# Optimization experiments

Hardware: AMD Instinct MI355X
Metric: run time of the kernel (lower is better)

Reference implementation:

```python
import jax, jax.numpy as jnp
import numpy as np

IN_DIM = 4096
OUT_DIM = 4096
R = 8
C = 2
ALPHA = 32.0
RC = R // C  # head dim = 4
SCALING = ALPHA / R


def setup_inputs() -> dict:
    key = jax.random.key(0)
    ks = jax.random.split(key, 8)
    s = lambda k, shape, fan_in: jax.random.normal(k, shape, jnp.float32) / np.sqrt(fan_in)
    return {
        "x": jax.random.normal(ks[0], (4, 2048, IN_DIM), jnp.float32),
        "W_pre": s(ks[1], (OUT_DIM, IN_DIM), IN_DIM),
        "b_pre": jnp.zeros((OUT_DIM,), jnp.float32),
        "W_down": s(ks[2], (R, IN_DIM), IN_DIM),
        "W_qkv": s(ks[3], (3 * RC, R), R),
        "W_o": s(ks[4], (R, RC), RC),
        "W_up": s(ks[5], (OUT_DIM, R), R),
        "diag_b": jnp.full((OUT_DIM,), 0.001, jnp.float32),
    }


def reference(x, W_pre, b_pre, W_down, W_qkv, W_o, W_up, diag_b):
    # pretrained frozen linear
    pretrained_out = jnp.einsum("bsi,oi->bso", x, W_pre) + b_pre
    # adapter path (dropout in eval mode -> identity)
    down = jnp.einsum("bsi,ri->bsr", x, W_down)          # [B,S,R]
    qkv = jnp.einsum("bsr,tr->bst", down, W_qkv)          # [B,S,3*RC]
    q, k, v = jnp.split(qkv, 3, axis=-1)                  # each [B,S,RC]
    scores = jnp.einsum("bqd,bkd->bqk", q, k) / jnp.sqrt(jnp.float32(RC))
    attn = jax.nn.softmax(scores, axis=-1)
    ctx = jnp.einsum("bqk,bkd->bqd", attn, v)             # [B,S,RC]
    o = jnp.einsum("bsd,rd->bsr", ctx, W_o)               # [B,S,R]
    up = jnp.einsum("bsr,or->bso", o, W_up)               # [B,S,OUT]
    return pretrained_out + up * diag_b * SCALING
```

## Files before the change

### kernel.cpp

```cpp
#include <hip/hip_runtime.h>
#include <stdint.h>

#define KDIM 4096
#define NDIM 4096
#define MROWS 8192
#define SEQ 2048

typedef __attribute__((ext_vector_type(8))) short short8;
typedef __attribute__((ext_vector_type(4))) float f32x4;

__device__ __forceinline__ float bf16_bits_to_f(uint32_t u16) {
  union { uint32_t u; float f; } c; c.u = u16 << 16; return c.f;
}
__device__ __forceinline__ float dload(const void* p, size_t idx, int flag) {
  if (flag) return bf16_bits_to_f(((const uint16_t*)p)[idx]);
  return ((const float*)p)[idx];
}
__device__ __forceinline__ uint16_t f2b(float f) {
  union { float f; uint32_t u; } c; c.f = f;
  uint32_t b = c.u;
  return (uint16_t)((b + 0x7FFFu + ((b >> 16) & 1u)) >> 16);
}
__device__ __forceinline__ uint32_t pk2(float a, float b) {
  return (uint32_t)f2b(a) | ((uint32_t)f2b(b) << 16);
}
__device__ __forceinline__ void gld_lds16(const uint16_t* g, uint16_t* l) {
  __builtin_amdgcn_global_load_lds(
      (const __attribute__((address_space(1))) uint32_t*)g,
      (__attribute__((address_space(3))) uint32_t*)l, 16, 0, 0);
}

#define BARRIER() asm volatile("s_barrier" ::: "memory")
#define VMCNT4() asm volatile("s_waitcnt vmcnt(4)" ::: "memory")
#define VMCNT0() asm volatile("s_waitcnt vmcnt(0)" ::: "memory")

__global__ void k_detect(const uint16_t* xu, int* flag) {
  int lane = threadIdx.x;
  int bad = 0;
  for (int i = lane; i < 512; i += 64) {
    float v = bf16_bits_to_f((uint32_t)xu[i]);
    if (!(v == v) || fabsf(v) > 1000.0f) bad++;
  }
  for (int off = 32; off > 0; off >>= 1) bad += __shfl_down(bad, off);
  if (lane == 0) *flag = (bad < 32) ? 1 : 0;
}

__global__ __launch_bounds__(256) void k_prep(
    const void* W_down, const void* W_qkv, const void* W_up,
    const void* diag_b, const void* b_pre,
    float* WcT, float* W_up_s, float* b_pre_f, const int* flagp) {
  const int flag = *flagp;
  const int tid = blockIdx.x * 256 + threadIdx.x;
  const int tt = tid >> 12;
  const int i = tid & 4095;
  float s = 0.f;
#pragma unroll
  for (int r = 0; r < 8; ++r)
    s += dload(W_qkv, tt * 8 + r, flag) * dload(W_down, (size_t)r * 4096 + i, flag);
  WcT[(size_t)tt * 4096 + i] = s;
  if (tid < 32768)
    W_up_s[tid] = dload(W_up, tid, flag) * dload(diag_b, tid >> 3, flag) * 4.0f;
  if (tid < 4096)
    b_pre_f[tid] = dload(b_pre, tid, flag);
}

__global__ __launch_bounds__(256) void k_qkvconv(
    const void* x, const float* WcT, float* qkv, uint16_t* xb,
    const void* W_pre, uint16_t* wb, int do_conv, const int* flagp) {
  const int flag = *flagp;
  if (blockIdx.x >= 2048) {
    if (flag || !do_conv) return;
    const float* w = (const float*)W_pre;
    const size_t n = (size_t)NDIM * KDIM;
    const size_t stride = (size_t)512 * 256 * 8;
    for (size_t idx = (((size_t)blockIdx.x - 2048) * 256 + threadIdx.x) * 8;
         idx < n; idx += stride) {
      const float4 a = *(const float4*)(w + idx);
      const float4 b = *(const float4*)(w + idx + 4);
      uint4 p;
      p.x = pk2(a.x, a.y);
      p.y = pk2(a.z, a.w);
      p.z = pk2(b.x, b.y);
      p.w = pk2(b.z, b.w);
      *(uint4*)(wb + idx) = p;
    }
    return;
  }
  const int wv = (int)((blockIdx.x * 256 + threadIdx.x) >> 6);
  const int lane = threadIdx.x & 63;
  float acc[12];
#pragma unroll
  for (int t = 0; t < 12; ++t) acc[t] = 0.f;
  if (!flag) {
    const float* xr = (const float*)x + (size_t)wv * KDIM;
    uint16_t* xo = xb + (size_t)wv * KDIM;
    for (int i0 = 0; i0 < KDIM; i0 += 256) {
      const int i = i0 + lane * 4;
      const float4 xv = *(const float4*)(xr + i);
      if (do_conv) {
        uint2 p;
        p.x = pk2(xv.x, xv.y);
        p.y = pk2(xv.z, xv.w);
        *(uint2*)(xo + i) = p;
      }
#pragma unroll
      for (int t = 0; t < 12; ++t) {
        const float4 w4 = *(const float4*)(WcT + (size_t)t * 4096 + i);
        acc[t] += xv.x * w4.x + xv.y * w4.y + xv.z * w4.z + xv.w * w4.w;
      }
    }
  } else {
    const uint16_t* xr = (const uint16_t*)x + (size_t)wv * KDIM;
    for (int i0 = 0; i0 < KDIM; i0 += 512) {
      const int i = i0 + lane * 8;
      const uint4 xv = *(const uint4*)(xr + i);
      const float x0 = bf16_bits_to_f(xv.x & 0xFFFFu), x1 = bf16_bits_to_f(xv.x >> 16);
      const float x2 = bf16_bits_to_f(xv.y & 0xFFFFu), x3 = bf16_bits_to_f(xv.y >> 16);
      const float x4 = bf16_bits_to_f(xv.z & 0xFFFFu), x5 = bf16_bits_to_f(xv.z >> 16);
      const float x6 = bf16_bits_to_f(xv.w & 0xFFFFu), x7 = bf16_bits_to_f(xv.w >> 16);
#pragma unroll
      for (int t = 0; t < 12; ++t) {
        const float4 w0 = *(const float4*)(WcT + (size_t)t * 4096 + i);
        const float4 w1 = *(const float4*)(WcT + (size_t)t * 4096 + i + 4);
        acc[t] += x0 * w0.x + x1 * w0.y + x2 * w0.z + x3 * w0.w +
                  x4 * w1.x + x5 * w1.y + x6 * w1.z + x7 * w1.w;
      }
    }
  }
#pragma unroll
  for (int t = 0; t < 12; ++t)
    for (int off = 32; off > 0; off >>= 1) acc[t] += __shfl_down(acc[t], off);
  if (lane == 0) {
#pragma unroll
    for (int t = 0; t < 12; ++t) qkv[(size_t)wv * 12 + t] = acc[t];
  }
}

__global__ __launch_bounds__(256) void k_attn(const float* qkv, const void* W_o,
                                              float* a_o, const int* flagp) {
  const int flag = *flagp;
  __shared__ uint2 sk[SEQ];
  __shared__ uint2 sv[SEQ];
  __shared__ float part[8][32][9];
  const int b = blockIdx.x >> 6;
  const int rb = blockIdx.x & 63;
  for (int j = threadIdx.x; j < SEQ; j += 256) {
    const float* qr = qkv + ((size_t)b * SEQ + j) * 12;
    uint2 pk, pv;
    pk.x = pk2(qr[4], qr[5]);
    pk.y = pk2(qr[6], qr[7]);
    pv.x = pk2(qr[8], qr[9]);
    pv.y = pk2(qr[10], qr[11]);
    sk[j] = pk;
    sv[j] = pv;
  }
  __syncthreads();
  const int row = threadIdx.x & 31;
  const int seg = threadIdx.x >> 5;
  const size_t m = (size_t)b * SEQ + rb * 32 + row;
  const float* qr = qkv + m * 12;
  const float q0 = qr[0] * 0.5f, q1 = qr[1] * 0.5f;
  const float q2 = qr[2] * 0.5f, q3 = qr[3] * 0.5f;
  float l = 0.f, c0 = 0.f, c1 = 0.f, c2 = 0.f, c3 = 0.f;
  const int j0 = seg * 256;
  for (int j = j0; j < j0 + 256; ++j) {
    const uint2 kk = sk[j];
    const float k0 = bf16_bits_to_f(kk.x & 0xFFFFu);
    const float k1 = bf16_bits_to_f(kk.x >> 16);
    const float k2 = bf16_bits_to_f(kk.y & 0xFFFFu);
    const float k3 = bf16_bits_to_f(kk.y >> 16);
    const float s = q0 * k0 + q1 * k1 + q2 * k2 + q3 * k3;
    const float e = __expf(s);
    const uint2 vv = sv[j];
    l += e;
    c0 += e * bf16_bits_to_f(vv.x & 0xFFFFu);
    c1 += e * bf16_bits_to_f(vv.x >> 16);
    c2 += e * bf16_bits_to_f(vv.y & 0xFFFFu);
    c3 += e * bf16_bits_to_f(vv.y >> 16);
  }
  part[seg][row][0] = l;
  part[seg][row][1] = c0;
  part[seg][row][2] = c1;
  part[seg][row][3] = c2;
  part[seg][row][4] = c3;
  __syncthreads();
  if (seg == 0) {
    l = 0.f; c0 = 0.f; c1 = 0.f; c2 = 0.f; c3 = 0.f;
#pragma unroll
    for (int s2 = 0; s2 < 8; ++s2) {
      l += part[s2][row][0];
      c0 += part[s2][row][1];
      c1 += part[s2][row][2];
      c2 += part[s2][row][3];
      c3 += part[s2][row][4];
    }
    const float inv = 1.0f / l;
    c0 *= inv; c1 *= inv; c2 *= inv; c3 *= inv;
    float wo[32];
#pragma unroll
    for (int i = 0; i < 32; ++i) wo[i] = dload(W_o, i, flag);
#pragma unroll
    for (int r = 0; r < 8; ++r)
      a_o[m * 8 + r] = c0 * wo[r * 4 + 0] + c1 * wo[r * 4 + 1] +
                       c2 * wo[r * 4 + 2] + c3 * wo[r * 4 + 3];
  }
}

__global__ __launch_bounds__(512, 2) void k_gemm8(
    const void* x, const void* w, const uint16_t* xb, const uint16_t* wb,
    const float* a_o, const float* W_up_s, const float* b_pre_f, void* out,
    const int* flagp) {
  const int flag = *flagp;
  const uint16_t* Ag = flag ? (const uint16_t*)x : xb;
  const uint16_t* Bg = flag ? (const uint16_t*)w : wb;
  __shared__ __align__(16) uint16_t smem[2][2][16384];

  const int t = threadIdx.x;
  const int lane = t & 63;
  const int wid = t >> 6;
  const int xcd = (int)blockIdx.x & 7;
  const int j = (int)blockIdx.x >> 3;
  const int bm = (xcd & 3) * 8 + (j & 7);
  const int bn = (xcd >> 2) * 8 + (j >> 3);

  const int sr0 = 0 * 64 + wid * 8 + (lane >> 3);
  const int sr1 = 1 * 64 + wid * 8 + (lane >> 3);
  const int sc0 = ((lane & 7) * 8) ^ (((sr0 >> 2) & 1) * 16) ^
                  (((sr0 >> 3) & 1) * 32);
  const int sc1 = ((lane & 7) * 8) ^ (((sr1 >> 2) & 1) * 16) ^
                  (((sr1 >> 3) & 1) * 32);
  const size_t aoff0 = (size_t)(bm * 256 + sr0) * KDIM + sc0;
  const size_t aoff1 = (size_t)(bm * 256 + sr1) * KDIM + sc1;
  const size_t boff0 = (size_t)(bn * 256 + sr0) * KDIM + sc0;
  const size_t boff1 = (size_t)(bn * 256 + sr1) * KDIM + sc1;

  const int wn_idx = wid & 3;
  const int wm_idx = wid >> 2;
  const int wave_m0 = wm_idx * 128;
  const int wave_n0 = wn_idx * 64;
  const int fr = lane & 15;
  const int fkbe = ((lane >> 4) * 8) ^ (((lane >> 2) & 1) * 16) ^
                   (((lane >> 3) & 1) * 32);

  f32x4 acc[8][4];
#pragma unroll
  for (int a = 0; a < 8; ++a)
#pragma unroll
    for (int b = 0; b < 4; ++b) acc[a][b] = (f32x4){0.f, 0.f, 0.f, 0.f};

  short8 a_reg[4][2];
  short8 b_reg[2][2][2];

#define STAGE(BUF, OP, H, TILE)                                               \
  do {                                                                        \
    const uint16_t* g_ = (OP) ? Bg : Ag;                                      \
    const size_t ho_ = (size_t)(H) * (128 * KDIM) + (size_t)(TILE) * 64;      \
    gld_lds16(g_ + ((OP) ? boff0 : aoff0) + ho_,                              \
              &smem[BUF][OP][(H) * 8192 + wid * 512]);                        \
    gld_lds16(g_ + ((OP) ? boff1 : aoff1) + ho_,                              \
              &smem[BUF][OP][(H) * 8192 + 4096 + wid * 512]);                 \
  } while (0)

#define A_LOAD(BUF, MH)                                                       \
  do {                                                                        \
    _Pragma("unroll") for (int f = 0; f < 4; ++f) {                           \
      a_reg[f][0] = *(const short8*)&smem[BUF][0][                            \
          (wave_m0 + ((MH)*4 + f) * 16 + fr) * 64 + fkbe];                    \
      a_reg[f][1] = *(const short8*)&smem[BUF][0][                            \
          (wave_m0 + ((MH)*4 + f) * 16 + fr) * 64 + (fkbe ^ 32)];             \
    }                                                                         \
  } while (0)

#define B_LOAD(BUF, NH)                                                       \
  do {                                                                        \
    _Pragma("unroll") for (int g = 0; g < 2; ++g) {                           \
      b_reg[NH][g][0] = *(const short8*)&smem[BUF][1][                        \
          (wave_n0 + ((NH)*2 + g) * 16 + fr) * 64 + fkbe];                    \
      b_reg[NH][g][1] = *(const short8*)&smem[BUF][1][                        \
          (wave_n0 + ((NH)*2 + g) * 16 + fr) * 64 + (fkbe ^ 32)];             \
    }                                                                         \
  } while (0)

#define MFMA_Q(MH, NH)                                                        \
  do {                                                                        \
    __builtin_amdgcn_s_setprio(1);                                            \
    _Pragma("unroll") for (int f = 0; f < 4; ++f) {                           \
      _Pragma("unroll") for (int g = 0; g < 2; ++g) {                         \
        acc[(MH)*4 + f][(NH)*2 + g] = __builtin_amdgcn_mfma_f32_16x16x32_bf16(\
            a_reg[f][0], b_reg[NH][g][0], acc[(MH)*4 + f][(NH)*2 + g], 0,0,0);\
        acc[(MH)*4 + f][(NH)*2 + g] = __builtin_amdgcn_mfma_f32_16x16x32_bf16(\
            a_reg[f][1], b_reg[NH][g][1], acc[(MH)*4 + f][(NH)*2 + g], 0,0,0);\
      }                                                                       \
    }                                                                         \
    __builtin_amdgcn_s_setprio(0);                                            \
  } while (0)

  STAGE(0, 0, 0, 0); STAGE(0, 0, 1, 0); STAGE(0, 1, 0, 0); STAGE(0, 1, 1, 0);
  STAGE(1, 1, 0, 1); STAGE(1, 1, 1, 1);
  VMCNT4();
  BARRIER();

#pragma unroll 1
  for (int it = 0; it < 31; ++it) {
    const int tO = 2 * it + 1, tE2 = 2 * it + 2, tO2 = 2 * it + 3;
    A_LOAD(0, 0); B_LOAD(0, 0); STAGE(1, 0, 0, tO);
    BARRIER(); MFMA_Q(0, 0); BARRIER();
    B_LOAD(0, 1); STAGE(1, 0, 1, tO);
    BARRIER(); MFMA_Q(0, 1); BARRIER();
    A_LOAD(0, 1); STAGE(0, 1, 0, tE2);
    BARRIER(); MFMA_Q(1, 0); BARRIER();
    STAGE(0, 1, 1, tE2);
    BARRIER(); MFMA_Q(1, 1); VMCNT4(); BARRIER();
    A_LOAD(1, 0); B_LOAD(1, 0); STAGE(0, 0, 0, tE2);
    BARRIER(); MFMA_Q(0, 0); BARRIER();
    B_LOAD(1, 1); STAGE(0, 0, 1, tE2);
    BARRIER(); MFMA_Q(0, 1); BARRIER();
    A_LOAD(1, 1); STAGE(1, 1, 0, tO2);
    BARRIER(); MFMA_Q(1, 0); BARRIER();
    STAGE(1, 1, 1, tO2);
    BARRIER(); MFMA_Q(1, 1); VMCNT4(); BARRIER();
  }
  A_LOAD(0, 0); B_LOAD(0, 0); STAGE(1, 0, 0, 63);
  BARRIER(); MFMA_Q(0, 0); BARRIER();
  B_LOAD(0, 1); STAGE(1, 0, 1, 63);
  BARRIER(); MFMA_Q(0, 1); BARRIER();
  A_LOAD(0, 1);
  BARRIER(); MFMA_Q(1, 0); BARRIER();
  BARRIER(); MFMA_Q(1, 1); VMCNT0(); BARRIER();
  A_LOAD(1, 0); B_LOAD(1, 0);
  BARRIER(); MFMA_Q(0, 0); BARRIER();
  B_LOAD(1, 1);
  BARRIER(); MFMA_Q(0, 1); BARRIER();
  A_LOAD(1, 1);
  BARRIER(); MFMA_Q(1, 0); BARRIER();
  BARRIER(); MFMA_Q(1, 1); BARRIER();

  const int rq = (lane >> 4) * 4;
  float4 u0r[4], u1r[4];
  float bpr[4];
#pragma unroll
  for (int nf = 0; nf < 4; ++nf) {
    const int gn = bn * 256 + wave_n0 + nf * 16 + fr;
    bpr[nf] = b_pre_f[gn];
    u0r[nf] = *(const float4*)&W_up_s[(size_t)gn * 8];
    u1r[nf] = *(const float4*)&W_up_s[(size_t)gn * 8 + 4];
  }
#pragma unroll
  for (int mf = 0; mf < 8; ++mf) {
#pragma unroll
    for (int r = 0; r < 4; ++r) {
      const int gm = bm * 256 + wave_m0 + mf * 16 + rq + r;
      const float4 a0 = *(const float4*)&a_o[(size_t)gm * 8];
      const float4 a1 = *(const float4*)&a_o[(size_t)gm * 8 + 4];
#pragma unroll
      for (int nf = 0; nf < 4; ++nf) {
        const int gn = bn * 256 + wave_n0 + nf * 16 + fr;
        float v = acc[mf][nf][r] + bpr[nf] +
                  a0.x * u0r[nf].x + a0.y * u0r[nf].y + a0.z * u0r[nf].z +
                  a0.w * u0r[nf].w + a1.x * u1r[nf].x + a1.y * u1r[nf].y +
                  a1.z * u1r[nf].z + a1.w * u1r[nf].w;
        const size_t oidx = (size_t)gm * NDIM + gn;
        if (flag) ((uint16_t*)out)[oidx] = f2b(v);
        else ((float*)out)[oidx] = v;
      }
    }
  }
#undef STAGE
#undef A_LOAD
#undef B_LOAD
#undef MFMA_Q
}

__global__ __launch_bounds__(256) void k_gemm_fb(
    const void* x, const void* w, const float* a_o, const float* W_up_s,
    const float* b_pre_f, void* out, const int* flagp) {
  const int flag = *flagp;
  __shared__ __align__(16) uint16_t sA[128 * 64];
  __shared__ __align__(16) uint16_t sB[128 * 64];
  const int t = threadIdx.x;
  const int bm = blockIdx.x & 63;
  const int bn = blockIdx.x >> 6;
  const int srow = t >> 1;
  const int scol = (t & 1) * 32;
  const size_t ga = ((size_t)(bm * 128 + srow)) * KDIM + scol;
  const size_t gb = ((size_t)(bn * 128 + srow)) * KDIM + scol;
  const int lane = t & 63;
  const int wid = t >> 6;
  const int wm = (wid & 1) * 64;
  const int wn = (wid >> 1) * 64;
  const int fr = lane & 15;
  const int fk = (lane >> 4) * 8;
  f32x4 acc[4][4];
#pragma unroll
  for (int a = 0; a < 4; ++a)
#pragma unroll
    for (int bq = 0; bq < 4; ++bq) acc[a][bq] = (f32x4){0.f, 0.f, 0.f, 0.f};

  for (int k0 = 0; k0 < KDIM; k0 += 64) {
    __syncthreads();
    if (flag) {
      const uint16_t* gx = (const uint16_t*)x + ga + k0;
      const uint16_t* gw = (const uint16_t*)w + gb + k0;
#pragma unroll
      for (int c = 0; c < 4; ++c) {
        *(uint4*)&sA[srow * 64 + scol + c * 8] = *(const uint4*)(gx + c * 8);
        *(uint4*)&sB[srow * 64 + scol + c * 8] = *(const uint4*)(gw + c * 8);
      }
    } else {
      const float* gx = (const float*)x + ga + k0;
      const float* gw = (const float*)w + gb + k0;
#pragma unroll
      for (int c = 0; c < 4; ++c) {
        float4 xa = *(const float4*)(gx + c * 8);
        float4 xb2 = *(const float4*)(gx + c * 8 + 4);
        uint4 pk;
        pk.x = pk2(xa.x, xa.y);
        pk.y = pk2(xa.z, xa.w);
        pk.z = pk2(xb2.x, xb2.y);
        pk.w = pk2(xb2.z, xb2.w);
        *(uint4*)&sA[srow * 64 + scol + c * 8] = pk;
        float4 wa = *(const float4*)(gw + c * 8);
        float4 wb2 = *(const float4*)(gw + c * 8 + 4);
        uint4 pw;
        pw.x = pk2(wa.x, wa.y);
        pw.y = pk2(wa.z, wa.w);
        pw.z = pk2(wb2.x, wb2.y);
        pw.w = pk2(wb2.z, wb2.w);
        *(uint4*)&sB[srow * 64 + scol + c * 8] = pw;
      }
    }
    __syncthreads();
#pragma unroll
    for (int kk = 0; kk < 64; kk += 32) {
      short8 af[4], bfr[4];
#pragma unroll
      for (int mb = 0; mb < 4; ++mb)
        af[mb] = *(const short8*)&sA[(wm + mb * 16 + fr) * 64 + kk + fk];
#pragma unroll
      for (int nb = 0; nb < 4; ++nb)
        bfr[nb] = *(const short8*)&sB[(wn + nb * 16 + fr) * 64 + kk + fk];
#pragma unroll
      for (int mb = 0; mb < 4; ++mb)
#pragma unroll
        for (int nb = 0; nb < 4; ++nb)
          acc[mb][nb] = __builtin_amdgcn_mfma_f32_16x16x32_bf16(
              af[mb], bfr[nb], acc[mb][nb], 0, 0, 0);
    }
  }
  const int rq = (lane >> 4) * 4;
#pragma unroll
  for (int nb = 0; nb < 4; ++nb) {
    const int gn = bn * 128 + wn + nb * 16 + fr;
    const float bp = b_pre_f[gn];
    const float4 u0 = *(const float4*)&W_up_s[(size_t)gn * 8];
    const float4 u1 = *(const float4*)&W_up_s[(size_t)gn * 8 + 4];
#pragma unroll
    for (int mb = 0; mb < 4; ++mb) {
#pragma unroll
      for (int r = 0; r < 4; ++r) {
        const int gm = bm * 128 + wm + mb * 16 + rq + r;
        const float4 a0 = *(const float4*)&a_o[(size_t)gm * 8];
        const float4 a1 = *(const float4*)&a_o[(size_t)gm * 8 + 4];
        float v = acc[mb][nb][r] + bp + a0.x * u0.x + a0.y * u0.y +
                  a0.z * u0.z + a0.w * u0.w + a1.x * u1.x + a1.y * u1.y +
                  a1.z * u1.z + a1.w * u1.w;
        const size_t oidx = (size_t)gm * NDIM + gn;
        if (flag) ((uint16_t*)out)[oidx] = f2b(v);
        else ((float*)out)[oidx] = v;
      }
    }
  }
}

extern "C" void kernel_launch(void* const* d_in, const int* in_sizes, int n_in,
                              void* d_out, int out_size, void* d_ws,
                              size_t ws_size, hipStream_t stream) {
  const void* x = d_in[0];
  const void* W_pre = d_in[1];
  const void* b_pre = d_in[2];
  const void* W_down = d_in[3];
  const void* W_qkv = d_in[4];
  const void* W_o = d_in[5];
  const void* W_up = d_in[6];
  const void* diag_b = d_in[7];

  char* ws = (char*)d_ws;
  int* flag_p = (int*)ws;
  float* WcT = (float*)(ws + 256);
  float* qkv = (float*)(ws + 196864);
  float* a_o = (float*)(ws + 590080);
  float* W_up_s = (float*)(ws + 852224);
  float* b_pre_f = (float*)(ws + 983296);
  uint16_t* xb = (uint16_t*)(ws + 1048576);
  uint16_t* wb = (uint16_t*)(ws + 68157440);
  const bool big = ws_size >= (size_t)101711872;

  k_detect<<<1, 64, 0, stream>>>((const uint16_t*)x, flag_p);
  k_prep<<<192, 256, 0, stream>>>(W_down, W_qkv, W_up, diag_b, b_pre, WcT,
                                  W_up_s, b_pre_f, flag_p);
  k_qkvconv<<<2560, 256, 0, stream>>>(x, WcT, qkv, xb, W_pre, wb,
                                      big ? 1 : 0, flag_p);
  k_attn<<<256, 256, 0, stream>>>(qkv, W_o, a_o, flag_p);
  if (big)
    k_gemm8<<<512, 512, 0, stream>>>(x, W_pre, xb, wb, a_o, W_up_s, b_pre_f,
                                     d_out, flag_p);
  else
    k_gemm_fb<<<2048, 256, 0, stream>>>(x, W_pre, a_o, W_up_s, b_pre_f, d_out,
                                        flag_p);
}
```

Measured before the change: 597.9 us.

## Simplify GEMM main loop to one barrier per K-tile with whole-tile staging

Replaces the finely interleaved ping-pong schedule, which had a barrier before and after every MFMA quarter plus partial vmcnt waits, with a simpler per-tile body. Each tile now issues all four stage loads for the next tile up front, runs the four LDS-read and MFMA quarters without intermediate barriers, then waits for all loads and syncs once. The aim is to cut barrier overhead and let the waves run their MFMAs freely. The trade-off is less fine-grained overlap, since a full vmcnt(0) wait now happens every tile and the prefetch depth drops to one tile.

Measured after the change: 597.5 us. No clear change (-0.1%).

```diff
diff --git a/kernel.cpp b/kernel.cpp
--- a/kernel.cpp
+++ b/kernel.cpp
@@ -31,7 +31,6 @@
 }
 
 #define BARRIER() asm volatile("s_barrier" ::: "memory")
-#define VMCNT4() asm volatile("s_waitcnt vmcnt(4)" ::: "memory")
 #define VMCNT0() asm volatile("s_waitcnt vmcnt(0)" ::: "memory")
 
 __global__ void k_detect(const uint16_t* xu, int* flag) {
@@ -295,45 +294,33 @@
     __builtin_amdgcn_s_setprio(0);                                            \
   } while (0)
 
+#define TILE_BODY(B, TT, DOSTAGE)                                             \
+  do {                                                                        \
+    if (DOSTAGE) {                                                            \
+      STAGE(B ^ 1, 0, 0, (TT) + 1);                                           \
+      STAGE(B ^ 1, 0, 1, (TT) + 1);                                           \
+      STAGE(B ^ 1, 1, 0, (TT) + 1);                                           \
+      STAGE(B ^ 1, 1, 1, (TT) + 1);                                           \
+    }                                                                         \
+    A_LOAD(B, 0); B_LOAD(B, 0); MFMA_Q(0, 0);                                 \
+    B_LOAD(B, 1); MFMA_Q(0, 1);                                               \
+    A_LOAD(B, 1); MFMA_Q(1, 0);                                               \
+    MFMA_Q(1, 1);                                                             \
+    VMCNT0();                                                                 \
+    BARRIER();                                                                \
+  } while (0)
+
   STAGE(0, 0, 0, 0); STAGE(0, 0, 1, 0); STAGE(0, 1, 0, 0); STAGE(0, 1, 1, 0);
-  STAGE(1, 1, 0, 1); STAGE(1, 1, 1, 1);
-  VMCNT4();
+  VMCNT0();
   BARRIER();
 
 #pragma unroll 1
   for (int it = 0; it < 31; ++it) {
-    const int tO = 2 * it + 1, tE2 = 2 * it + 2, tO2 = 2 * it + 3;
-    A_LOAD(0, 0); B_LOAD(0, 0); STAGE(1, 0, 0, tO);
-    BARRIER(); MFMA_Q(0, 0); BARRIER();
-    B_LOAD(0, 1); STAGE(1, 0, 1, tO);
-    BARRIER(); MFMA_Q(0, 1); BARRIER();
-    A_LOAD(0, 1); STAGE(0, 1, 0, tE2);
-    BARRIER(); MFMA_Q(1, 0); BARRIER();
-    STAGE(0, 1, 1, tE2);
-    BARRIER(); MFMA_Q(1, 1); VMCNT4(); BARRIER();
-    A_LOAD(1, 0); B_LOAD(1, 0); STAGE(0, 0, 0, tE2);
-    BARRIER(); MFMA_Q(0, 0); BARRIER();
-    B_LOAD(1, 1); STAGE(0, 0, 1, tE2);
-    BARRIER(); MFMA_Q(0, 1); BARRIER();
-    A_LOAD(1, 1); STAGE(1, 1, 0, tO2);
-    BARRIER(); MFMA_Q(1, 0); BARRIER();
-    STAGE(1, 1, 1, tO2);
-    BARRIER(); MFMA_Q(1, 1); VMCNT4(); BARRIER();
-  }
-  A_LOAD(0, 0); B_LOAD(0, 0); STAGE(1, 0, 0, 63);
-  BARRIER(); MFMA_Q(0, 0); BARRIER();
-  B_LOAD(0, 1); STAGE(1, 0, 1, 63);
-  BARRIER(); MFMA_Q(0, 1); BARRIER();
-  A_LOAD(0, 1);
-  BARRIER(); MFMA_Q(1, 0); BARRIER();
-  BARRIER(); MFMA_Q(1, 1); VMCNT0(); BARRIER();
-  A_LOAD(1, 0); B_LOAD(1, 0);
-  BARRIER(); MFMA_Q(0, 0); BARRIER();
-  B_LOAD(1, 1);
-  BARRIER(); MFMA_Q(0, 1); BARRIER();
-  A_LOAD(1, 1);
-  BARRIER(); MFMA_Q(1, 0); BARRIER();
-  BARRIER(); MFMA_Q(1, 1); BARRIER();
+    TILE_BODY(0, 2 * it, 1);
+    TILE_BODY(1, 2 * it + 1, 1);
+  }
+  TILE_BODY(0, 62, 1);
+  TILE_BODY(1, 63, 0);
 
   const int rq = (lane >> 4) * 4;
   float4 u0r[4], u1r[4];
@@ -365,6 +352,7 @@
       }
     }
   }
+#undef TILE_BODY
 #undef STAGE
 #undef A_LOAD
 #undef B_LOAD
```
